# Performance work log

Measured on AMD Instinct MI355X. Metric: run time of the kernel, lower is better.

The kernel has to match this reference:

```python
import jax, jax.numpy as jnp
import numpy as np

N, D, D_QK, D_V = 8192, 1024, 128, 128

def setup_inputs() -> dict:
    key = jax.random.key(0)
    k1, k2, k3, k4 = jax.random.split(key, 4)
    s = 1.0 / np.sqrt(D)
    return {
        "x": jax.random.normal(k1, (N, D), dtype=jnp.float32),
        "Wq": jax.random.normal(k2, (D_QK, D), dtype=jnp.float32) * s,
        "Wk": jax.random.normal(k3, (D_QK, D), dtype=jnp.float32) * s,
        "Wv": jax.random.normal(k4, (D_V, D), dtype=jnp.float32) * s,
    }

def reference(x, Wq, Wk, Wv):
    # NOTE: original code MULTIPLIES by sqrt(D_qk) (dq_sqrt_inv = np.sqrt(D_qk)).
    scale = jnp.sqrt(jnp.asarray(D_QK, dtype=x.dtype))
    q = x @ Wq.T            # [N, D_qk]
    k = x @ Wk.T            # [N, D_qk]
    v = x @ Wv.T            # [N, D_v]
    scores = scale * (q @ k.T)          # [N, N]
    attn = jax.nn.softmax(scores, axis=-1)
    return attn @ v          # [N, D_v]
```

## Files before the change

kernel.cpp:

```cpp
#include <hip/hip_runtime.h>
#include <hip/hip_bf16.h>
#include <math.h>
#include <stdint.h>

#define N_TOK 8192
#define D_IN  1024
#define D_H   128
#define SPLIT 8

typedef __bf16 bf16;
typedef __attribute__((ext_vector_type(4))) __bf16 bf16x4;
typedef __attribute__((ext_vector_type(8))) __bf16 bf16x8;
typedef __attribute__((ext_vector_type(4))) float floatx4;

#define MFMA16(a, b, c) __builtin_amdgcn_mfma_f32_16x16x32_bf16((a), (b), (c), 0, 0, 0)

#define QSCALE 16.322625246404958f

#define RESCALE_THR 8.0f

__device__ __forceinline__ uint32_t pack2(float a, float b) {
    union { bf16 h[2]; uint32_t u; } z;
    z.h[0] = (bf16)a; z.h[1] = (bf16)b; return z.u;
}

__device__ __forceinline__ size_t vtf_idx(int n, int d) {
    return ((size_t)((n >> 6) * 8 + (d >> 4)) << 10)
         + (((n >> 3) & 7) << 7) + ((d & 15) << 3) + (n & 7);
}
__device__ __forceinline__ size_t khf_idx(int n, int d) {
    return ((size_t)(((n >> 6) * 4 + (d >> 5)) * 4 + ((n >> 4) & 3)) << 9)
         + (((d >> 3) & 3) << 7) + ((n & 15) << 3) + (d & 7);
}

#define X_OCT (N_TOK * D_IN / 8)
#define W_OCT (3 * D_H * D_IN / 8)

__global__ __launch_bounds__(256)
void convert_kernel(const float* __restrict__ x,
                    const float* __restrict__ Wq,
                    const float* __restrict__ Wk,
                    const float* __restrict__ Wv,
                    bf16* __restrict__ xhf, bf16* __restrict__ xlf,
                    bf16* __restrict__ whf, bf16* __restrict__ wlf)
{
    const int gid = blockIdx.x * 256 + threadIdx.x;
    const float* src;
    bf16 *dh, *dl;
    size_t doff;
    if (gid < X_OCT) {
        int lane = gid & 63, fc = gid >> 6;
        int kc = fc & 31, mt = fc >> 5;
        int n  = mt * 16 + (lane & 15);
        int k0 = kc * 32 + ((lane >> 4) << 3);
        src = x + (size_t)n * D_IN + k0;
        dh = xhf; dl = xlf; doff = (size_t)gid << 3;
    } else {
        int w = gid - X_OCT;
        int y = w >> 14, r = w & 16383;
        int lane = r & 63, fc = r >> 6;
        int kc = fc & 31, ct = fc >> 5;
        int col = ct * 16 + (lane & 15);
        int k0  = kc * 32 + ((lane >> 4) << 3);
        const float* W = (y == 0) ? Wq : (y == 1) ? Wk : Wv;
        src = W + (size_t)col * D_IN + k0;
        dh = whf; dl = wlf; doff = (size_t)w << 3;
    }
    float4 a = *(const float4*)src;
    float4 b = *(const float4*)(src + 4);
    float vv[8] = { a.x, a.y, a.z, a.w, b.x, b.y, b.z, b.w };
    bf16x8 h, l;
    #pragma unroll
    for (int j = 0; j < 8; ++j) {
        bf16 hh = (bf16)vv[j];
        h[j] = hh;
        l[j] = (bf16)(vv[j] - (float)hh);
    }
    *(bf16x8*)(dh + doff) = h;
    *(bf16x8*)(dl + doff) = l;
}

__global__ __launch_bounds__(256, 2)
void qkv_kernel(const bf16* __restrict__ xhf, const bf16* __restrict__ xlf,
                const bf16* __restrict__ whf, const bf16* __restrict__ wlf,
                bf16* __restrict__ q_hi, bf16* __restrict__ q_lo,
                bf16* __restrict__ khf, bf16* __restrict__ klf,
                bf16* __restrict__ vtf)
{
    __shared__ bf16 w_s[2][16384];

    const int t    = threadIdx.x;
    const int lane = t & 63;
    const int wid  = t >> 6;
    const int wr   = wid >> 1;
    const int wc   = wid & 1;
    const int lid  = lane & 15;
    const int quad = lane >> 4;
    const int m0   = blockIdx.x * 64;
    const bf16* wh = whf + ((size_t)blockIdx.y << 17);
    const bf16* wl = wlf + ((size_t)blockIdx.y << 17);

    auto stage = [&](int c0, int buf) {
        #pragma unroll
        for (int i = 0; i < 8; ++i) {
            int p   = wid * 8 + i;
            int hl  = p >> 4, ct = (p >> 1) & 7, kci = p & 1;
            const bf16* src = (hl ? wl : wh)
                            + ((size_t)(ct * 32 + c0 + kci) << 9) + (lane << 3);
            bf16* dst = &w_s[buf][p << 9];
            __builtin_amdgcn_global_load_lds(
                (const __attribute__((address_space(1))) void*)src,
                (__attribute__((address_space(3))) void*)dst, 16, 0, 0);
        }
    };

    floatx4 acc[2][4];
    #pragma unroll
    for (int m = 0; m < 2; ++m)
        #pragma unroll
        for (int ct = 0; ct < 4; ++ct)
            #pragma unroll
            for (int r = 0; r < 4; ++r) acc[m][ct][r] = 0.f;

#define LOADX(Hh0, Ll0, Hh1, Ll1, cc)                                       \
    {                                                                       \
        _Pragma("unroll")                                                   \
        for (int m = 0; m < 2; ++m) {                                       \
            int mt = (m0 >> 4) + wr * 2 + m;                                \
            const size_t xb = ((size_t)(mt * 32 + (cc) * 2) << 9) + (lane << 3); \
            Hh0[m] = *(const bf16x8*)(xhf + xb);                            \
            Ll0[m] = *(const bf16x8*)(xlf + xb);                            \
            Hh1[m] = *(const bf16x8*)(xhf + xb + 512);                      \
            Ll1[m] = *(const bf16x8*)(xlf + xb + 512);                      \
        }                                                                   \
    }

#define COMPUTE(Hh0, Ll0, Hh1, Ll1, cbuf)                                   \
    {                                                                       \
        _Pragma("unroll")                                                   \
        for (int kci = 0; kci < 2; ++kci) {                                 \
            _Pragma("unroll")                                               \
            for (int ct = 0; ct < 4; ++ct) {                                \
                const int pb = (((wc * 4 + ct) * 2 + kci) << 9) + (lane << 3); \
                bf16x8 bh = *(const bf16x8*)&w_s[cbuf][pb];                 \
                bf16x8 bl = *(const bf16x8*)&w_s[cbuf][(16 << 9) + pb];     \
                _Pragma("unroll")                                           \
                for (int m = 0; m < 2; ++m) {                               \
                    bf16x8 xh = kci ? Hh1[m] : Hh0[m];                      \
                    bf16x8 xl = kci ? Ll1[m] : Ll0[m];                      \
                    acc[m][ct] = MFMA16(xh, bh, acc[m][ct]);                \
                    acc[m][ct] = MFMA16(xl, bh, acc[m][ct]);                \
                    acc[m][ct] = MFMA16(xh, bl, acc[m][ct]);                \
                }                                                           \
            }                                                               \
        }                                                                   \
    }

    bf16x8 Ah0[2], Al0[2], Ah1[2], Al1[2];
    bf16x8 Bh0[2], Bl0[2], Bh1[2], Bl1[2];

    stage(0, 0);
    LOADX(Ah0, Al0, Ah1, Al1, 0);

    for (int c = 0; c < 16; c += 2) {
        __syncthreads();
        stage((c + 1) * 2, 1);
        LOADX(Bh0, Bl0, Bh1, Bl1, c + 1);
        COMPUTE(Ah0, Al0, Ah1, Al1, 0);
        __syncthreads();
        if (c < 14) {
            stage((c + 2) * 2, 0);
            LOADX(Ah0, Al0, Ah1, Al1, c + 2);
        }
        COMPUTE(Bh0, Bl0, Bh1, Bl1, 1);
    }

#undef LOADX
#undef COMPUTE

    if (blockIdx.y == 0) {
        #pragma unroll
        for (int s2 = 0; s2 < 2; ++s2)
            #pragma unroll
            for (int ct = 0; ct < 4; ++ct)
                #pragma unroll
                for (int r = 0; r < 4; ++r) {
                    int row = m0 + wr * 32 + s2 * 16 + quad * 4 + r;
                    int col = wc * 64 + ct * 16 + lid;
                    float a = acc[s2][ct][r] * QSCALE;
                    bf16 h = (bf16)a;
                    q_hi[(size_t)row * D_H + col] = h;
                    q_lo[(size_t)row * D_H + col] = (bf16)(a - (float)h);
                }
    } else if (blockIdx.y == 1) {
        #pragma unroll
        for (int s2 = 0; s2 < 2; ++s2)
            #pragma unroll
            for (int ct = 0; ct < 4; ++ct)
                #pragma unroll
                for (int r = 0; r < 4; ++r) {
                    int n = m0 + wr * 32 + s2 * 16 + quad * 4 + r;
                    int d = wc * 64 + ct * 16 + lid;
                    float a = acc[s2][ct][r];
                    bf16 h = (bf16)a;
                    size_t idx = khf_idx(n, d);
                    khf[idx] = h;
                    klf[idx] = (bf16)(a - (float)h);
                }
    } else {
        #pragma unroll
        for (int s2 = 0; s2 < 2; ++s2)
            #pragma unroll
            for (int ct = 0; ct < 4; ++ct)
                #pragma unroll
                for (int r = 0; r < 4; ++r) {
                    int n = m0 + wr * 32 + s2 * 16 + quad * 4 + r;
                    int d = wc * 64 + ct * 16 + lid;
                    vtf[vtf_idx(n, d)] = (bf16)acc[s2][ct][r];
                }
    }
}

#define BQ   128
#define BKEY 64

__global__ __launch_bounds__(256, 2)
void flash_kernel(const bf16* __restrict__ qh, const bf16* __restrict__ ql,
                  const bf16* __restrict__ khf, const bf16* __restrict__ klf,
                  const bf16* __restrict__ vtf,
                  bf16*  __restrict__ opart,
                  float* __restrict__ mpart,
                  float* __restrict__ lpart)
{
    __shared__ bf16 k_s[2][16384];

    const int t     = threadIdx.x;
    const int lane  = t & 63;
    const int wid   = t >> 6;
    const int lid   = lane & 15;
    const int quad  = lane >> 4;
    const int q0    = blockIdx.x * BQ;
    const int strip = wid * 32;
    const int sp    = blockIdx.y;
    const int tile0 = sp * (N_TOK / BKEY / SPLIT);
    const int tile1 = tile0 + (N_TOK / BKEY / SPLIT);

    bf16x8 b_hi[2][4], b_lo[2][4];
    #pragma unroll
    for (int ct = 0; ct < 2; ++ct) {
        const size_t rowb = (size_t)(q0 + strip + ct * 16 + lid) * D_H + quad * 8;
        #pragma unroll
        for (int kc = 0; kc < 4; ++kc) {
            b_hi[ct][kc] = *(const bf16x8*)(qh + rowb + kc * 32);
            b_lo[ct][kc] = *(const bf16x8*)(ql + rowb + kc * 32);
        }
    }

    bf16x8 vones;
    #pragma unroll
    for (int j = 0; j < 8; ++j) vones[j] = (bf16)1.0f;

    float m_run[2] = { -INFINITY, -INFINITY };
    floatx4 l_acc[2];
    #pragma unroll
    for (int ct = 0; ct < 2; ++ct)
        #pragma unroll
        for (int r = 0; r < 4; ++r) l_acc[ct][r] = 0.f;
    floatx4 o_acc[8][2];
    #pragma unroll
    for (int dt = 0; dt < 8; ++dt)
        #pragma unroll
        for (int ct = 0; ct < 2; ++ct)
            #pragma unroll
            for (int r = 0; r < 4; ++r) o_acc[dt][ct][r] = 0.f;

    auto stage = [&](int tile, int buf) {
        const bf16* gh = khf + ((size_t)tile << 13) + (wid << 11) + (lane << 3);
        const bf16* gl = klf + ((size_t)tile << 13) + (wid << 11) + (lane << 3);
        bf16* lh = &k_s[buf][wid << 11];
        bf16* ll = lh + 8192;
        #pragma unroll
        for (int i = 0; i < 4; ++i) {
            __builtin_amdgcn_global_load_lds(
                (const __attribute__((address_space(1))) void*)(gh + i * 512),
                (__attribute__((address_space(3))) void*)(lh + i * 512), 16, 0, 0);
            __builtin_amdgcn_global_load_lds(
                (const __attribute__((address_space(1))) void*)(gl + i * 512),
                (__attribute__((address_space(3))) void*)(ll + i * 512), 16, 0, 0);
        }
    };

    stage(tile0, 0);

    for (int tt = tile0; tt < tile1; ++tt) {
        const int cb = (tt - tile0) & 1;
        __syncthreads();
        if (tt + 1 < tile1) stage(tt + 1, cb ^ 1);

        const bf16* khp = &k_s[cb][0];
        const bf16* klp = &k_s[cb][8192];
        floatx4 s[4][2];
        #pragma unroll
        for (int mt = 0; mt < 4; ++mt)
            #pragma unroll
            for (int ct = 0; ct < 2; ++ct)
                #pragma unroll
                for (int r = 0; r < 4; ++r) s[mt][ct][r] = 0.f;

        __builtin_amdgcn_s_setprio(1);
        #pragma unroll
        for (int kc = 0; kc < 4; ++kc)
            #pragma unroll
            for (int mt = 0; mt < 4; ++mt) {
                const int fo = ((kc * 4 + mt) << 9) + (lane << 3);
                bf16x8 ah = *(const bf16x8*)&khp[fo];
                bf16x8 al = *(const bf16x8*)&klp[fo];
                #pragma unroll
                for (int ct = 0; ct < 2; ++ct) {
                    s[mt][ct] = MFMA16(ah, b_hi[ct][kc], s[mt][ct]);
                    s[mt][ct] = MFMA16(al, b_hi[ct][kc], s[mt][ct]);
                    s[mt][ct] = MFMA16(ah, b_lo[ct][kc], s[mt][ct]);
                }
            }
        __builtin_amdgcn_s_setprio(0);

        const bf16* vb = vtf + ((size_t)tt << 13) + (lane << 3);
        bf16x8 vf0[8];
        #pragma unroll
        for (int dt = 0; dt < 8; ++dt)
            vf0[dt] = *(const bf16x8*)(vb + ((size_t)dt << 10));

        float mx[2];
        #pragma unroll
        for (int ct = 0; ct < 2; ++ct) {
            float a0 = fmaxf(s[0][ct][0], s[0][ct][1]);
            float a1 = fmaxf(s[0][ct][2], s[0][ct][3]);
            float a2 = fmaxf(s[1][ct][0], s[1][ct][1]);
            float a3 = fmaxf(s[1][ct][2], s[1][ct][3]);
            float a4 = fmaxf(s[2][ct][0], s[2][ct][1]);
            float a5 = fmaxf(s[2][ct][2], s[2][ct][3]);
            float a6 = fmaxf(s[3][ct][0], s[3][ct][1]);
            float a7 = fmaxf(s[3][ct][2], s[3][ct][3]);
            float b0 = fmaxf(fmaxf(a0, a1), fmaxf(a2, a3));
            float b1 = fmaxf(fmaxf(a4, a5), fmaxf(a6, a7));
            float c0 = fmaxf(b0, b1);
            c0 = fmaxf(c0, __shfl_xor(c0, 16, 64));
            c0 = fmaxf(c0, __shfl_xor(c0, 32, 64));
            mx[ct] = c0;
        }

        const bool need = __any((mx[0] - m_run[0] > RESCALE_THR) ||
                                (mx[1] - m_run[1] > RESCALE_THR));
        float alpha[2] = { 1.f, 1.f };
        if (need) {
            #pragma unroll
            for (int ct = 0; ct < 2; ++ct) {
                float mn = fmaxf(m_run[ct], mx[ct]);
                alpha[ct] = exp2f(m_run[ct] - mn);
                m_run[ct] = mn;
            }
        }

        uint32_t u0[4][2], u1[4][2];
        #pragma unroll
        for (int ct = 0; ct < 2; ++ct)
            #pragma unroll
            for (int mt = 0; mt < 4; ++mt) {
                float p0 = exp2f(s[mt][ct][0] - m_run[ct]);
                float p1 = exp2f(s[mt][ct][1] - m_run[ct]);
                float p2 = exp2f(s[mt][ct][2] - m_run[ct]);
                float p3 = exp2f(s[mt][ct][3] - m_run[ct]);
                u0[mt][ct] = pack2(p0, p1);
                u1[mt][ct] = pack2(p2, p3);
            }

        bf16x8 pB[2][2];
        {
            const int lsrc = ((quad & 1) << 5) + lid;
            const bool himt = (quad & 2) != 0;
            #pragma unroll
            for (int kc2 = 0; kc2 < 2; ++kc2)
                #pragma unroll
                for (int ct = 0; ct < 2; ++ct) {
                    const int mA = kc2 * 2, mB = kc2 * 2 + 1;
                    uint32_t w0a = __shfl((int)u0[mA][ct], lsrc, 64);
                    uint32_t w0b = __shfl((int)u0[mB][ct], lsrc, 64);
                    uint32_t w1a = __shfl((int)u1[mA][ct], lsrc, 64);
                    uint32_t w1b = __shfl((int)u1[mB][ct], lsrc, 64);
                    uint32_t w2a = __shfl((int)u0[mA][ct], lsrc + 16, 64);
                    uint32_t w2b = __shfl((int)u0[mB][ct], lsrc + 16, 64);
                    uint32_t w3a = __shfl((int)u1[mA][ct], lsrc + 16, 64);
                    uint32_t w3b = __shfl((int)u1[mB][ct], lsrc + 16, 64);
                    union { uint32_t w[4]; bf16x8 v; } z;
                    z.w[0] = himt ? w0b : w0a;
                    z.w[1] = himt ? w1b : w1a;
                    z.w[2] = himt ? w2b : w2a;
                    z.w[3] = himt ? w3b : w3a;
                    pB[kc2][ct] = z.v;
                }
        }

        bf16x8 vf1[8];
        #pragma unroll
        for (int dt = 0; dt < 8; ++dt)
            vf1[dt] = *(const bf16x8*)(vb + ((size_t)dt << 10) + 512);

        if (need) {
            #pragma unroll
            for (int ct = 0; ct < 2; ++ct) {
                #pragma unroll
                for (int r = 0; r < 4; ++r) l_acc[ct][r] *= alpha[ct];
                #pragma unroll
                for (int dt = 0; dt < 8; ++dt)
                    #pragma unroll
                    for (int r = 0; r < 4; ++r)
                        o_acc[dt][ct][r] *= alpha[ct];
            }
        }

        __builtin_amdgcn_s_setprio(1);
        #pragma unroll
        for (int ct = 0; ct < 2; ++ct) {
            l_acc[ct] = MFMA16(vones, pB[0][ct], l_acc[ct]);
            l_acc[ct] = MFMA16(vones, pB[1][ct], l_acc[ct]);
        }
        #pragma unroll
        for (int dt = 0; dt < 8; ++dt)
            #pragma unroll
            for (int ct = 0; ct < 2; ++ct) {
                o_acc[dt][ct] = MFMA16(vf0[dt], pB[0][ct], o_acc[dt][ct]);
                o_acc[dt][ct] = MFMA16(vf1[dt], pB[1][ct], o_acc[dt][ct]);
            }
        __builtin_amdgcn_s_setprio(0);
    }

    uint32_t* opw = (uint32_t*)(opart + (size_t)sp * N_TOK * D_H);
    #pragma unroll
    for (int dt = 0; dt < 8; ++dt)
        #pragma unroll
        for (int ct = 0; ct < 2; ++ct) {
            int qrow  = q0 + strip + ct * 16 + lid;
            int dbase = dt * 16 + quad * 4;
            opw[(qrow * D_H + dbase) >> 1]     = pack2(o_acc[dt][ct][0], o_acc[dt][ct][1]);
            opw[(qrow * D_H + dbase + 2) >> 1] = pack2(o_acc[dt][ct][2], o_acc[dt][ct][3]);
        }
    if (quad == 0) {
        #pragma unroll
        for (int ct = 0; ct < 2; ++ct) {
            int row = q0 + strip + ct * 16 + lid;
            mpart[(size_t)sp * N_TOK + row] = m_run[ct];
            lpart[(size_t)sp * N_TOK + row] = l_acc[ct][0];
        }
    }
}

__global__ __launch_bounds__(256)
void combine_kernel(const bf16* __restrict__ opart,
                    const float* __restrict__ mpart,
                    const float* __restrict__ lpart,
                    float* __restrict__ out)
{
    const int t   = threadIdx.x;
    const int row = blockIdx.x * 16 + (t >> 4);
    const int c0  = (t & 15) * 8;

    float ms[SPLIT], ls[SPLIT];
    float mstar = -INFINITY;
    #pragma unroll
    for (int s = 0; s < SPLIT; ++s) {
        ms[s] = mpart[(size_t)s * N_TOK + row];
        ls[s] = lpart[(size_t)s * N_TOK + row];
        mstar = fmaxf(mstar, ms[s]);
    }
    float acc[8] = {};
    float L = 0.f;
    #pragma unroll
    for (int s = 0; s < SPLIT; ++s) {
        float w = exp2f(ms[s] - mstar);
        L += w * ls[s];
        bf16x8 o = *(const bf16x8*)&opart[((size_t)s * N_TOK + row) * D_H + c0];
        #pragma unroll
        for (int j = 0; j < 8; ++j)
            acc[j] += w * (float)o[j];
    }
    float inv = 1.f / L;
    float* dst = &out[(size_t)row * D_H + c0];
    *(float4*)(dst + 0) = make_float4(acc[0] * inv, acc[1] * inv,
                                      acc[2] * inv, acc[3] * inv);
    *(float4*)(dst + 4) = make_float4(acc[4] * inv, acc[5] * inv,
                                      acc[6] * inv, acc[7] * inv);
}

extern "C" void kernel_launch(void* const* d_in, const int* in_sizes, int n_in,
                              void* d_out, int out_size, void* d_ws, size_t ws_size,
                              hipStream_t stream) {
    const float* x  = (const float*)d_in[0];
    const float* Wq = (const float*)d_in[1];
    const float* Wk = (const float*)d_in[2];
    const float* Wv = (const float*)d_in[3];
    float* out = (float*)d_out;

    bf16* wsb = (bf16*)d_ws;
    const size_t SZ = (size_t)N_TOK * D_H;
    bf16* xhf = wsb;
    bf16* xlf = xhf + (size_t)X_OCT * 8;
    bf16* whf = xlf + (size_t)X_OCT * 8;
    bf16* wlf = whf + (size_t)W_OCT * 8;
    bf16* qh  = wlf + (size_t)W_OCT * 8;
    bf16* ql  = qh + SZ;
    bf16* khf = ql + SZ;
    bf16* klf = khf + SZ;
    bf16* vtf = klf + SZ;
    bf16* opart = vtf + SZ;
    float* mpart = (float*)(opart + (size_t)SPLIT * SZ);
    float* lpart = mpart + (size_t)SPLIT * N_TOK;

    convert_kernel<<<dim3((X_OCT + W_OCT) / 256), 256, 0, stream>>>(
        x, Wq, Wk, Wv, xhf, xlf, whf, wlf);
    qkv_kernel<<<dim3(N_TOK / 64, 3), 256, 0, stream>>>(
        xhf, xlf, whf, wlf, qh, ql, khf, klf, vtf);
    flash_kernel<<<dim3(N_TOK / BQ, SPLIT), 256, 0, stream>>>(
        qh, ql, khf, klf, vtf, opart, mpart, lpart);
    combine_kernel<<<dim3(N_TOK / 16), 256, 0, stream>>>(opart, mpart, lpart, out);
}
```

Baseline: 193.3 us.

## Fuse x fp32-to-bf16 hi/lo split into QKV projection kernel

The convert kernel no longer converts x. The QKV kernel now loads fp32 x directly and splits it into bf16 hi/lo parts in registers before the MFMAs. This removes a full write and re-read of two bf16 copies of x (32 MB of traffic) and a kernel pass. In exchange, each of the three blockIdx.y projection blocks reloads fp32 x and repeats the conversion, so x reads triple and register pressure rises from the float4 prefetch buffers.

```diff
diff --git a/kernel.cpp b/kernel.cpp
--- a/kernel.cpp
+++ b/kernel.cpp
@@ -24,64 +24,52 @@
     z.h[0] = (bf16)a; z.h[1] = (bf16)b; return z.u;
 }
 
-__device__ __forceinline__ size_t vtf_idx(int n, int d) {
-    return ((size_t)((n >> 6) * 8 + (d >> 4)) << 10)
-         + (((n >> 3) & 7) << 7) + ((d & 15) << 3) + (n & 7);
-}
-__device__ __forceinline__ size_t khf_idx(int n, int d) {
-    return ((size_t)(((n >> 6) * 4 + (d >> 5)) * 4 + ((n >> 4) & 3)) << 9)
-         + (((d >> 3) & 3) << 7) + ((n & 15) << 3) + (d & 7);
-}
-
-#define X_OCT (N_TOK * D_IN / 8)
-#define W_OCT (3 * D_H * D_IN / 8)
-
-__global__ __launch_bounds__(256)
-void convert_kernel(const float* __restrict__ x,
-                    const float* __restrict__ Wq,
-                    const float* __restrict__ Wk,
-                    const float* __restrict__ Wv,
-                    bf16* __restrict__ xhf, bf16* __restrict__ xlf,
-                    bf16* __restrict__ whf, bf16* __restrict__ wlf)
-{
-    const int gid = blockIdx.x * 256 + threadIdx.x;
-    const float* src;
-    bf16 *dh, *dl;
-    size_t doff;
-    if (gid < X_OCT) {
-        int lane = gid & 63, fc = gid >> 6;
-        int kc = fc & 31, mt = fc >> 5;
-        int n  = mt * 16 + (lane & 15);
-        int k0 = kc * 32 + ((lane >> 4) << 3);
-        src = x + (size_t)n * D_IN + k0;
-        dh = xhf; dl = xlf; doff = (size_t)gid << 3;
-    } else {
-        int w = gid - X_OCT;
-        int y = w >> 14, r = w & 16383;
-        int lane = r & 63, fc = r >> 6;
-        int kc = fc & 31, ct = fc >> 5;
-        int col = ct * 16 + (lane & 15);
-        int k0  = kc * 32 + ((lane >> 4) << 3);
-        const float* W = (y == 0) ? Wq : (y == 1) ? Wk : Wv;
-        src = W + (size_t)col * D_IN + k0;
-        dh = whf; dl = wlf; doff = (size_t)w << 3;
-    }
-    float4 a = *(const float4*)src;
-    float4 b = *(const float4*)(src + 4);
+__device__ __forceinline__ void cvt8(float4 a, float4 b, bf16x8& h, bf16x8& l) {
     float vv[8] = { a.x, a.y, a.z, a.w, b.x, b.y, b.z, b.w };
-    bf16x8 h, l;
     #pragma unroll
     for (int j = 0; j < 8; ++j) {
         bf16 hh = (bf16)vv[j];
         h[j] = hh;
         l[j] = (bf16)(vv[j] - (float)hh);
     }
-    *(bf16x8*)(dh + doff) = h;
-    *(bf16x8*)(dl + doff) = l;
+}
+
+__device__ __forceinline__ size_t vtf_idx(int n, int d) {
+    return ((size_t)((n >> 6) * 8 + (d >> 4)) << 10)
+         + (((n >> 3) & 7) << 7) + ((d & 15) << 3) + (n & 7);
+}
+__device__ __forceinline__ size_t khf_idx(int n, int d) {
+    return ((size_t)(((n >> 6) * 4 + (d >> 5)) * 4 + ((n >> 4) & 3)) << 9)
+         + (((d >> 3) & 3) << 7) + ((n & 15) << 3) + (d & 7);
+}
+
+#define W_OCT (3 * D_H * D_IN / 8)
+
+__global__ __launch_bounds__(256)
+void convert_kernel(const float* __restrict__ Wq,
+                    const float* __restrict__ Wk,
+                    const float* __restrict__ Wv,
+                    bf16* __restrict__ whf, bf16* __restrict__ wlf)
+{
+    const int w = blockIdx.x * 256 + threadIdx.x;
+    int y = w >> 14, r = w & 16383;
+    int lane = r & 63, fc = r >> 6;
+    int kc = fc & 31, ct = fc >> 5;
+    int col = ct * 16 + (lane & 15);
+    int k0  = kc * 32 + ((lane >> 4) << 3);
+    const float* W = (y == 0) ? Wq : (y == 1) ? Wk : Wv;
+    const float* src = W + (size_t)col * D_IN + k0;
+    float4 a = *(const float4*)src;
+    float4 b = *(const float4*)(src + 4);
+    bf16x8 h, l;
+    cvt8(a, b, h, l);
+    size_t doff = (size_t)w << 3;
+    *(bf16x8*)(whf + doff) = h;
+    *(bf16x8*)(wlf + doff) = l;
 }
 
 __global__ __launch_bounds__(256, 2)
-void qkv_kernel(const bf16* __restrict__ xhf, const bf16* __restrict__ xlf,
+void qkv_kernel(const float* __restrict__ x,
                 const bf16* __restrict__ whf, const bf16* __restrict__ wlf,
                 bf16* __restrict__ q_hi, bf16* __restrict__ q_lo,
                 bf16* __restrict__ khf, bf16* __restrict__ klf,
@@ -122,20 +110,32 @@
             #pragma unroll
             for (int r = 0; r < 4; ++r) acc[m][ct][r] = 0.f;
 
-#define LOADX(Hh0, Ll0, Hh1, Ll1, cc)                                       \
+    float4 FA[8], FB[8];
+    bf16x8 Xh0[2], Xl0[2], Xh1[2], Xl1[2];
+
+#define LOADF(F, cc)                                                        \
     {                                                                       \
         _Pragma("unroll")                                                   \
         for (int m = 0; m < 2; ++m) {                                       \
-            int mt = (m0 >> 4) + wr * 2 + m;                                \
-            const size_t xb = ((size_t)(mt * 32 + (cc) * 2) << 9) + (lane << 3); \
-            Hh0[m] = *(const bf16x8*)(xhf + xb);                            \
-            Ll0[m] = *(const bf16x8*)(xlf + xb);                            \
-            Hh1[m] = *(const bf16x8*)(xhf + xb + 512);                      \
-            Ll1[m] = *(const bf16x8*)(xlf + xb + 512);                      \
+            int n = m0 + wr * 32 + m * 16 + (lane & 15);                    \
+            const float* xs = x + (size_t)n * D_IN + (cc) * 64              \
+                            + ((lane >> 4) << 3);                           \
+            F[m * 4 + 0] = *(const float4*)xs;                              \
+            F[m * 4 + 1] = *(const float4*)(xs + 4);                        \
+            F[m * 4 + 2] = *(const float4*)(xs + 32);                       \
+            F[m * 4 + 3] = *(const float4*)(xs + 36);                       \
         }                                                                   \
     }
 
-#define COMPUTE(Hh0, Ll0, Hh1, Ll1, cbuf)                                   \
+#define CONVX(F)                                                            \
+    {                                                                       \
+        cvt8(F[0], F[1], Xh0[0], Xl0[0]);                                   \
+        cvt8(F[2], F[3], Xh1[0], Xl1[0]);                                   \
+        cvt8(F[4], F[5], Xh0[1], Xl0[1]);                                   \
+        cvt8(F[6], F[7], Xh1[1], Xl1[1]);                                   \
+    }
+
+#define COMPUTE(cbuf)                                                       \
     {                                                                       \
         _Pragma("unroll")                                                   \
         for (int kci = 0; kci < 2; ++kci) {                                 \
@@ -146,8 +146,8 @@
                 bf16x8 bl = *(const bf16x8*)&w_s[cbuf][(16 << 9) + pb];     \
                 _Pragma("unroll")                                           \
                 for (int m = 0; m < 2; ++m) {                               \
-                    bf16x8 xh = kci ? Hh1[m] : Hh0[m];                      \
-                    bf16x8 xl = kci ? Ll1[m] : Ll0[m];                      \
+                    bf16x8 xh = kci ? Xh1[m] : Xh0[m];                      \
+                    bf16x8 xl = kci ? Xl1[m] : Xl0[m];                      \
                     acc[m][ct] = MFMA16(xh, bh, acc[m][ct]);                \
                     acc[m][ct] = MFMA16(xl, bh, acc[m][ct]);                \
                     acc[m][ct] = MFMA16(xh, bl, acc[m][ct]);                \
@@ -156,26 +156,26 @@
         }                                                                   \
     }
 
-    bf16x8 Ah0[2], Al0[2], Ah1[2], Al1[2];
-    bf16x8 Bh0[2], Bl0[2], Bh1[2], Bl1[2];
-
     stage(0, 0);
-    LOADX(Ah0, Al0, Ah1, Al1, 0);
+    LOADF(FA, 0);
 
     for (int c = 0; c < 16; c += 2) {
         __syncthreads();
         stage((c + 1) * 2, 1);
-        LOADX(Bh0, Bl0, Bh1, Bl1, c + 1);
-        COMPUTE(Ah0, Al0, Ah1, Al1, 0);
+        LOADF(FB, c + 1);
+        CONVX(FA);
+        COMPUTE(0);
         __syncthreads();
         if (c < 14) {
             stage((c + 2) * 2, 0);
-            LOADX(Ah0, Al0, Ah1, Al1, c + 2);
-        }
-        COMPUTE(Bh0, Bl0, Bh1, Bl1, 1);
-    }
-
-#undef LOADX
+            LOADF(FA, c + 2);
+        }
+        CONVX(FB);
+        COMPUTE(1);
+    }
+
+#undef LOADF
+#undef CONVX
 #undef COMPUTE
 
     if (blockIdx.y == 0) {
@@ -502,9 +502,7 @@
 
     bf16* wsb = (bf16*)d_ws;
     const size_t SZ = (size_t)N_TOK * D_H;
-    bf16* xhf = wsb;
-    bf16* xlf = xhf + (size_t)X_OCT * 8;
-    bf16* whf = xlf + (size_t)X_OCT * 8;
+    bf16* whf = wsb;
     bf16* wlf = whf + (size_t)W_OCT * 8;
     bf16* qh  = wlf + (size_t)W_OCT * 8;
     bf16* ql  = qh + SZ;
@@ -515,10 +513,10 @@
     float* mpart = (float*)(opart + (size_t)SPLIT * SZ);
     float* lpart = mpart + (size_t)SPLIT * N_TOK;
 
-    convert_kernel<<<dim3((X_OCT + W_OCT) / 256), 256, 0, stream>>>(
-        x, Wq, Wk, Wv, xhf, xlf, whf, wlf);
+    convert_kernel<<<dim3(W_OCT / 256), 256, 0, stream>>>(
+        Wq, Wk, Wv, whf, wlf);
     qkv_kernel<<<dim3(N_TOK / 64, 3), 256, 0, stream>>>(
-        xhf, xlf, whf, wlf, qh, ql, khf, klf, vtf);
+        x, whf, wlf, qh, ql, khf, klf, vtf);
     flash_kernel<<<dim3(N_TOK / BQ, SPLIT), 256, 0, stream>>>(
         qh, ql, khf, klf, vtf, opart, mpart, lpart);
     combine_kernel<<<dim3(N_TOK / 16), 256, 0, stream>>>(opart, mpart, lpart, out);
```

Result: slower. 198.4 us (+2.6%).
